# Kernel optimization log

Measured on AMD Instinct MI355X. Metric: run time of the kernel, lower is better.

The kernel has to match this reference:

```python
import jax, jax.numpy as jnp
import numpy as np

N = 50000      # nodes
E = 800000     # edges (avg degree 16)
G = 500        # graphs in batch
D = 128        # emb_dim
ED = 7         # edge_dim
L = 5          # num_layers
C = 10         # num_class
BN_EPS = 1e-5


def _bn(x, g, b, m, v):
    # BatchNorm1d in eval mode: running stats
    return (x - m) * jax.lax.rsqrt(v + BN_EPS) * g + b


def setup_inputs() -> dict:
    key = jax.random.key(0)
    ks = jax.random.split(key, 32)
    f32 = jnp.float32
    edge_attr = jax.random.normal(ks[0], (E, ED), f32)
    edge_index = jax.random.randint(ks[1], (2, E), 0, N)
    batch = jnp.sort(jax.random.randint(ks[2], (N,), 0, G))

    w = lambda k, shp, s: jax.random.normal(k, shp, f32) * s
    s_in = 1.0 / np.sqrt(D)
    node_emb = w(ks[3], (1, D), 1.0)
    edge_W = w(ks[4], (L, ED, D), 1.0 / np.sqrt(ED))
    edge_b = w(ks[5], (L, D), 0.01)
    mlp_W1 = w(ks[6], (L, D, D), s_in)
    mlp_b1 = w(ks[7], (L, D), 0.01)
    mlp_W2 = w(ks[8], (L, D, D), s_in)
    mlp_b2 = w(ks[9], (L, D), 0.01)
    bn1_g = jax.random.uniform(ks[10], (L, D), f32, 0.5, 1.5)
    bn1_b = w(ks[11], (L, D), 0.1)
    bn1_m = w(ks[12], (L, D), 0.1)
    bn1_v = jax.random.uniform(ks[13], (L, D), f32, 0.5, 1.5)
    bn2_g = jax.random.uniform(ks[14], (L, D), f32, 0.5, 1.5)
    bn2_b = w(ks[15], (L, D), 0.1)
    bn2_m = w(ks[16], (L, D), 0.1)
    bn2_v = jax.random.uniform(ks[17], (L, D), f32, 0.5, 1.5)
    head_W1 = w(ks[18], (D, D), s_in)
    head_b1 = w(ks[19], (D,), 0.01)
    head_W2 = w(ks[20], (D, C), s_in)
    head_b2 = w(ks[21], (C,), 0.01)
    return dict(edge_attr=edge_attr, edge_index=edge_index, batch=batch,
                node_emb=node_emb, edge_W=edge_W, edge_b=edge_b,
                mlp_W1=mlp_W1, mlp_b1=mlp_b1, bn1_g=bn1_g, bn1_b=bn1_b,
                bn1_m=bn1_m, bn1_v=bn1_v, mlp_W2=mlp_W2, mlp_b2=mlp_b2,
                bn2_g=bn2_g, bn2_b=bn2_b, bn2_m=bn2_m, bn2_v=bn2_v,
                head_W1=head_W1, head_b1=head_b1, head_W2=head_W2, head_b2=head_b2)


def reference(edge_attr, edge_index, batch, node_emb, edge_W, edge_b,
              mlp_W1, mlp_b1, bn1_g, bn1_b, bn1_m, bn1_v,
              mlp_W2, mlp_b2, bn2_g, bn2_b, bn2_m, bn2_v,
              head_W1, head_b1, head_W2, head_b2):
    src, dst = edge_index[0], edge_index[1]
    # node_emb indexed by zeros -> every node starts with the same row
    x = jnp.broadcast_to(node_emb[0], (N, D))
    for l in range(L):
        # GINEConv: msg_ij = relu(x_j + Lin(edge_attr_ij)); aggr = sum over in-edges
        e = edge_attr @ edge_W[l] + edge_b[l]               # [E, D]
        msg = jax.nn.relu(x[src] + e)                       # gather + add + relu
        agg = jax.ops.segment_sum(msg, dst, num_segments=N) # scatter-add
        h = x + agg                                         # (1 + eps) * x, eps = 0
        # inner MLP: Linear -> BN -> ReLU -> Linear
        h = h @ mlp_W1[l] + mlp_b1[l]
        h = jax.nn.relu(_bn(h, bn1_g[l], bn1_b[l], bn1_m[l], bn1_v[l]))
        h = h @ mlp_W2[l] + mlp_b2[l]
        # outer BN + ReLU (dropout identity in eval)
        x = jax.nn.relu(_bn(h, bn2_g[l], bn2_b[l], bn2_m[l], bn2_v[l]))
    # global mean pool over graphs
    counts = jnp.maximum(jax.ops.segment_sum(jnp.ones((N,), x.dtype), batch, num_segments=G), 1.0)
    g = jax.ops.segment_sum(x, batch, num_segments=G) / counts[:, None]
    # head: Linear -> ReLU -> (Dropout) -> Linear
    h = jax.nn.relu(g @ head_W1 + head_b1)
    return h @ head_W2 + head_b2
```

## Files before the change

kernel.cpp:

```cpp
#include <hip/hip_runtime.h>

#define N_NODES 50000
#define N_PAD   50048
#define N_EDGES 800000
#define N_GRAPHS 500
#define DIM 128
#define EDIM 7
#define LAYERS 5
#define NCLASS 10
#define BN_EPS 1e-5f
#define TM 64
#define AST 264
#define NSB ((N_NODES + 256) / 256)

typedef __attribute__((ext_vector_type(8))) short bf16x8;
typedef __attribute__((ext_vector_type(4))) float f32x4;
typedef _Float16 h2 __attribute__((ext_vector_type(2)));

struct __align__(32) ERec { uint4 ea; int src; int pad0, pad1, pad2; };

__device__ __forceinline__ unsigned short f2bf(float f) {
    unsigned u = __float_as_uint(f);
    u = u + 0x7fffu + ((u >> 16) & 1u);
    return (unsigned short)(u >> 16);
}
__device__ __forceinline__ float bf2f(unsigned short h) {
    return __uint_as_float(((unsigned)h) << 16);
}
__device__ __forceinline__ h2 u2h2(unsigned u) {
    union { unsigned u; h2 h; } c; c.u = u; return c.h;
}
__device__ __forceinline__ unsigned h22u(h2 h) {
    union { h2 h; unsigned u; } c; c.h = h; return c.u;
}
__device__ __forceinline__ unsigned packh2(float a, float b) {
    h2 h; h.x = (_Float16)a; h.y = (_Float16)b;
    return h22u(h);
}


__global__ void zero_ints(int* __restrict__ p, int n) {
    int i = blockIdx.x * 256 + threadIdx.x;
    if (i < n) p[i] = 0;
}

__global__ void hist_kernel(const int* __restrict__ dst, int* __restrict__ deg) {
    int e = blockIdx.x * 256 + threadIdx.x;
    if (e < N_EDGES) atomicAdd(&deg[dst[e]], 1);
}

__global__ __launch_bounds__(256)
void scan1(const int* __restrict__ deg, int* __restrict__ ro, int* __restrict__ bsums) {
    __shared__ int ws[4];
    int t = threadIdx.x;
    int i = blockIdx.x * 256 + t;
    int v = (i < N_NODES) ? deg[i] : 0;
    int lane = t & 63, wv = t >> 6;
    int s = v;
    #pragma unroll
    for (int off = 1; off < 64; off <<= 1) {
        int u = __shfl_up(s, off, 64);
        if (lane >= off) s += u;
    }
    if (lane == 63) ws[wv] = s;
    __syncthreads();
    if (t == 0) {
        int a = 0;
        #pragma unroll
        for (int k = 0; k < 4; ++k) { int x = ws[k]; ws[k] = a; a += x; }
        bsums[blockIdx.x] = a;
    }
    __syncthreads();
    int excl = s - v + ws[wv];
    if (i <= N_NODES) ro[i] = excl;
}

__global__ __launch_bounds__(256)
void scan2(int* __restrict__ bsums) {
    __shared__ int ws[4];
    int t = threadIdx.x;
    int v = (t < NSB) ? bsums[t] : 0;
    int lane = t & 63, wv = t >> 6;
    int s = v;
    #pragma unroll
    for (int off = 1; off < 64; off <<= 1) {
        int u = __shfl_up(s, off, 64);
        if (lane >= off) s += u;
    }
    if (lane == 63) ws[wv] = s;
    __syncthreads();
    if (t == 0) {
        int a = 0;
        #pragma unroll
        for (int k = 0; k < 4; ++k) { int x = ws[k]; ws[k] = a; a += x; }
    }
    __syncthreads();
    if (t < NSB) bsums[t] = s - v + ws[wv];
}

__global__ __launch_bounds__(256)
void scan3(int* __restrict__ ro, const int* __restrict__ bsums, int* __restrict__ cursor) {
    int i = blockIdx.x * 256 + threadIdx.x;
    if (i <= N_NODES) {
        int r = ro[i] + bsums[i >> 8];
        ro[i] = r;
        if (i < N_NODES) cursor[i] = r;
    }
}

__global__ void fill_rec(const int* __restrict__ dst, const int* __restrict__ src,
                         const float* __restrict__ edge_attr,
                         int* __restrict__ cursor, ERec* __restrict__ rec) {
    int e = blockIdx.x * 256 + threadIdx.x;
    if (e < N_EDGES) {
        const float* ap = edge_attr + (size_t)e * EDIM;
        uint4 ea;
        ea.x = packh2(ap[0], ap[1]);
        ea.y = packh2(ap[2], ap[3]);
        ea.z = packh2(ap[4], ap[5]);
        ea.w = packh2(ap[6], 0.f);
        int s = src[e];
        int pos = atomicAdd(&cursor[dst[e]], 1);
        rec[pos].ea = ea;
        rec[pos].src = s;
    }
}


__global__ void init_x(float* __restrict__ x, unsigned short* __restrict__ xb,
                       const float* __restrict__ emb) {
    int i = blockIdx.x * 256 + threadIdx.x;
    if (i < N_NODES * DIM) {
        float v = emb[i & (DIM - 1)];
        x[i] = v;
        xb[i] = f2bf(v);
    }
}

__global__ void prep_w(const float* __restrict__ W1, const float* __restrict__ W2,
                       unsigned short* __restrict__ Wthi, unsigned short* __restrict__ Wtlo) {
    int i = blockIdx.x * 256 + threadIdx.x;
    if (i >= 2 * LAYERS * DIM * DIM) return;
    int m = i >> 14;
    int n = i & 127;
    int k = (i >> 7) & 127;
    const float* W = (m < LAYERS) ? (W1 + (size_t)m * DIM * DIM)
                                  : (W2 + (size_t)(m - LAYERS) * DIM * DIM);
    float v = W[k * DIM + n];
    unsigned short hi = f2bf(v);
    float lo = v - bf2f(hi);
    size_t o = ((size_t)m << 14) + (size_t)n * DIM + k;
    Wthi[o] = hi;
    Wtlo[o] = f2bf(lo);
}


#if __has_builtin(__builtin_amdgcn_fdot2)
#define HAVE_FDOT2 1
#else
#define HAVE_FDOT2 0
#endif

__device__ __forceinline__ void edge_accum2(float& acc0, float& acc1,
                                            uint4 eav, unsigned xv,
                                            const unsigned* Wp0, const unsigned* Wp1,
                                            float b0, float b1) {
    float e0 = b0, e1 = b1;
#if HAVE_FDOT2
    e0 = __builtin_amdgcn_fdot2(u2h2(eav.x), u2h2(Wp0[0]), e0, false);
    e0 = __builtin_amdgcn_fdot2(u2h2(eav.y), u2h2(Wp0[1]), e0, false);
    e0 = __builtin_amdgcn_fdot2(u2h2(eav.z), u2h2(Wp0[2]), e0, false);
    e0 = __builtin_amdgcn_fdot2(u2h2(eav.w), u2h2(Wp0[3]), e0, false);
    e1 = __builtin_amdgcn_fdot2(u2h2(eav.x), u2h2(Wp1[0]), e1, false);
    e1 = __builtin_amdgcn_fdot2(u2h2(eav.y), u2h2(Wp1[1]), e1, false);
    e1 = __builtin_amdgcn_fdot2(u2h2(eav.z), u2h2(Wp1[2]), e1, false);
    e1 = __builtin_amdgcn_fdot2(u2h2(eav.w), u2h2(Wp1[3]), e1, false);
#else
    h2 ea01 = u2h2(eav.x), ea23 = u2h2(eav.y), ea45 = u2h2(eav.z), ea67 = u2h2(eav.w);
    float a[8] = {(float)ea01.x, (float)ea01.y, (float)ea23.x, (float)ea23.y,
                  (float)ea45.x, (float)ea45.y, (float)ea67.x, 0.f};
    #pragma unroll
    for (int kp = 0; kp < 4; ++kp) {
        h2 w0 = u2h2(Wp0[kp]), w1 = u2h2(Wp1[kp]);
        e0 += a[kp * 2] * (float)w0.x + a[kp * 2 + 1] * (float)w0.y;
        e1 += a[kp * 2] * (float)w1.x + a[kp * 2 + 1] * (float)w1.y;
    }
#endif
    acc0 += fmaxf(__uint_as_float(xv << 16)         + e0, 0.f);
    acc1 += fmaxf(__uint_as_float(xv & 0xffff0000u) + e1, 0.f);
}

__global__ __launch_bounds__(256, 8)
void aggregate(const float* __restrict__ x, const unsigned short* __restrict__ xb,
               float* __restrict__ h,
               const ERec* __restrict__ rec,
               const int* __restrict__ row_off,
               const float* __restrict__ eW, const float* __restrict__ eb) {
    int t = threadIdx.x;
    int wv = __builtin_amdgcn_readfirstlane(t >> 6);
    int lane = t & 63;
    int c0 = lane * 2;
    int n = blockIdx.x * 4 + wv;

    unsigned Wp0[4], Wp1[4];
    #pragma unroll
    for (int kp = 0; kp < 4; ++kp) {
        float w00 = eW[(kp * 2) * DIM + c0];
        float w01 = (kp * 2 + 1 < EDIM) ? eW[(kp * 2 + 1) * DIM + c0] : 0.f;
        float w10 = eW[(kp * 2) * DIM + c0 + 1];
        float w11 = (kp * 2 + 1 < EDIM) ? eW[(kp * 2 + 1) * DIM + c0 + 1] : 0.f;
        Wp0[kp] = packh2(w00, w01);
        Wp1[kp] = packh2(w10, w11);
    }
    float b0 = eb[c0], b1 = eb[c0 + 1];
    #pragma unroll
    for (int k = 0; k < 4; ++k) asm volatile("" : "+v"(Wp0[k]), "+v"(Wp1[k]));
    asm volatile("" : "+v"(b0), "+v"(b1));

    float acc0 = x[(size_t)n * DIM + c0];
    float acc1 = x[(size_t)n * DIM + c0 + 1];
    int idx = row_off[n], end = row_off[n + 1];

    for (; idx + 8 <= end; idx += 8) {
        ERec r[8];
        #pragma unroll
        for (int j = 0; j < 8; ++j) r[j] = rec[idx + j];
        unsigned xv[8];
        #pragma unroll
        for (int j = 0; j < 8; ++j)
            xv[j] = *reinterpret_cast<const unsigned*>(xb + (size_t)r[j].src * DIM + c0);
        #pragma unroll
        for (int j = 0; j < 8; ++j)
            edge_accum2(acc0, acc1, r[j].ea, xv[j], Wp0, Wp1, b0, b1);
    }
    for (; idx < end; ++idx) {
        ERec r0 = rec[idx];
        unsigned xv0 = *reinterpret_cast<const unsigned*>(xb + (size_t)r0.src * DIM + c0);
        edge_accum2(acc0, acc1, r0.ea, xv0, Wp0, Wp1, b0, b1);
    }

    float2 o; o.x = acc0; o.y = acc1;
    *reinterpret_cast<float2*>(h + (size_t)n * DIM + c0) = o;
}


__global__ __launch_bounds__(256)
void gemm2x(const float* __restrict__ in, float* __restrict__ outx,
            unsigned short* __restrict__ xb_out,
            const unsigned short* __restrict__ W1hi, const unsigned short* __restrict__ W1lo,
            const unsigned short* __restrict__ W2hi, const unsigned short* __restrict__ W2lo,
            const float* __restrict__ b1,
            const float* __restrict__ bn1g, const float* __restrict__ bn1b,
            const float* __restrict__ bn1m, const float* __restrict__ bn1v,
            const float* __restrict__ b2,
            const float* __restrict__ bn2g, const float* __restrict__ bn2b,
            const float* __restrict__ bn2m, const float* __restrict__ bn2v) {
    __shared__ __align__(16) unsigned short A2[TM * AST];
    int t = threadIdx.x;
    int r0 = blockIdx.x * TM;
    int w = t >> 6;
    int lane = t & 63;
    int q = lane >> 4;
    int l16 = lane & 15;

    bf16x8 bh[2][4], bl[2][4];
    #pragma unroll
    for (int nt = 0; nt < 2; ++nt) {
        int n = w * 32 + nt * 16 + l16;
        const bf16x8* gh = reinterpret_cast<const bf16x8*>(W1hi + (size_t)n * DIM);
        const bf16x8* gl = reinterpret_cast<const bf16x8*>(W1lo + (size_t)n * DIM);
        #pragma unroll
        for (int kc = 0; kc < 4; ++kc) {
            bh[nt][kc] = gh[kc * 4 + q];
            bl[nt][kc] = gl[kc * 4 + q];
        }
    }

    #pragma unroll
    for (int i = 0; i < 8; ++i) {
        int idx = t + i * 256;
        int row = idx >> 5;
        int kp = (idx & 31) * 4;
        float4 v = reinterpret_cast<const float4*>(in + (size_t)r0 * DIM)[idx];
        unsigned short h0 = f2bf(v.x), h1 = f2bf(v.y), h2_ = f2bf(v.z), h3 = f2bf(v.w);
        ushort4 hv; hv.x = h0; hv.y = h1; hv.z = h2_; hv.w = h3;
        ushort4 lv;
        lv.x = f2bf(v.x - bf2f(h0)); lv.y = f2bf(v.y - bf2f(h1));
        lv.z = f2bf(v.z - bf2f(h2_)); lv.w = f2bf(v.w - bf2f(h3));
        *reinterpret_cast<ushort4*>(&A2[row * AST + kp]) = hv;
        *reinterpret_cast<ushort4*>(&A2[row * AST + 128 + kp]) = lv;
    }
    __syncthreads();

    f32x4 acc[4][2];
    #pragma unroll
    for (int mt = 0; mt < 4; ++mt)
        #pragma unroll
        for (int nt = 0; nt < 2; ++nt)
            acc[mt][nt] = (f32x4){0.f, 0.f, 0.f, 0.f};

    #pragma unroll
    for (int kc = 0; kc < 4; ++kc) {
        bf16x8 ahi[4], alo[4];
        #pragma unroll
        for (int mt = 0; mt < 4; ++mt) {
            ahi[mt] = *reinterpret_cast<const bf16x8*>(&A2[(mt * 16 + l16) * AST + kc * 32 + q * 8]);
            alo[mt] = *reinterpret_cast<const bf16x8*>(&A2[(mt * 16 + l16) * AST + 128 + kc * 32 + q * 8]);
        }
        #pragma unroll
        for (int mt = 0; mt < 4; ++mt)
            #pragma unroll
            for (int nt = 0; nt < 2; ++nt) {
                acc[mt][nt] = __builtin_amdgcn_mfma_f32_16x16x32_bf16(ahi[mt], bh[nt][kc], acc[mt][nt], 0, 0, 0);
                acc[mt][nt] = __builtin_amdgcn_mfma_f32_16x16x32_bf16(ahi[mt], bl[nt][kc], acc[mt][nt], 0, 0, 0);
                acc[mt][nt] = __builtin_amdgcn_mfma_f32_16x16x32_bf16(alo[mt], bh[nt][kc], acc[mt][nt], 0, 0, 0);
            }
    }
    __syncthreads();

    #pragma unroll
    for (int nt = 0; nt < 2; ++nt) {
        int n = w * 32 + nt * 16 + l16;
        const bf16x8* gh = reinterpret_cast<const bf16x8*>(W2hi + (size_t)n * DIM);
        const bf16x8* gl = reinterpret_cast<const bf16x8*>(W2lo + (size_t)n * DIM);
        #pragma unroll
        for (int kc = 0; kc < 4; ++kc) {
            bh[nt][kc] = gh[kc * 4 + q];
            bl[nt][kc] = gl[kc * 4 + q];
        }
    }

    #pragma unroll
    for (int nt = 0; nt < 2; ++nt) {
        int col = w * 32 + nt * 16 + l16;
        float bias = b1[col];
        float sc = bn1g[col] * rsqrtf(bn1v[col] + BN_EPS);
        float sh = bn1b[col] - bn1m[col] * sc;
        #pragma unroll
        for (int mt = 0; mt < 4; ++mt) {
            #pragma unroll
            for (int r = 0; r < 4; ++r) {
                int rowl = mt * 16 + q * 4 + r;
                float o = fmaxf((acc[mt][nt][r] + bias) * sc + sh, 0.f);
                unsigned short hi = f2bf(o);
                A2[rowl * AST + col] = hi;
                A2[rowl * AST + 128 + col] = f2bf(o - bf2f(hi));
            }
        }
    }
    __syncthreads();

    #pragma unroll
    for (int mt = 0; mt < 4; ++mt)
        #pragma unroll
        for (int nt = 0; nt < 2; ++nt)
            acc[mt][nt] = (f32x4){0.f, 0.f, 0.f, 0.f};

    #pragma unroll
    for (int kc = 0; kc < 4; ++kc) {
        bf16x8 ahi[4], alo[4];
        #pragma unroll
        for (int mt = 0; mt < 4; ++mt) {
            ahi[mt] = *reinterpret_cast<const bf16x8*>(&A2[(mt * 16 + l16) * AST + kc * 32 + q * 8]);
            alo[mt] = *reinterpret_cast<const bf16x8*>(&A2[(mt * 16 + l16) * AST + 128 + kc * 32 + q * 8]);
        }
        #pragma unroll
        for (int mt = 0; mt < 4; ++mt)
            #pragma unroll
            for (int nt = 0; nt < 2; ++nt) {
                acc[mt][nt] = __builtin_amdgcn_mfma_f32_16x16x32_bf16(ahi[mt], bh[nt][kc], acc[mt][nt], 0, 0, 0);
                acc[mt][nt] = __builtin_amdgcn_mfma_f32_16x16x32_bf16(ahi[mt], bl[nt][kc], acc[mt][nt], 0, 0, 0);
                acc[mt][nt] = __builtin_amdgcn_mfma_f32_16x16x32_bf16(alo[mt], bh[nt][kc], acc[mt][nt], 0, 0, 0);
            }
    }

    #pragma unroll
    for (int nt = 0; nt < 2; ++nt) {
        int col = w * 32 + nt * 16 + l16;
        float bias = b2[col];
        float sc = bn2g[col] * rsqrtf(bn2v[col] + BN_EPS);
        float sh = bn2b[col] - bn2m[col] * sc;
        #pragma unroll
        for (int mt = 0; mt < 4; ++mt) {
            #pragma unroll
            for (int r = 0; r < 4; ++r) {
                int row = r0 + mt * 16 + q * 4 + r;
                float o = fmaxf((acc[mt][nt][r] + bias) * sc + sh, 0.f);
                outx[(size_t)row * DIM + col] = o;
                xb_out[(size_t)row * DIM + col] = f2bf(o);
            }
        }
    }
}


__global__ __launch_bounds__(256)
void pool_kernel(const float* __restrict__ x, const int* __restrict__ batch,
                 float* __restrict__ g) {
    __shared__ float sh[256];
    __shared__ int sb[2];
    int gid = blockIdx.x;
    int t = threadIdx.x;
    if (t < 2) {
        int tgt = gid + t;
        int lo = 0, hi = N_NODES;
        while (lo < hi) { int mid = (lo + hi) >> 1; if (batch[mid] < tgt) lo = mid + 1; else hi = mid; }
        sb[t] = lo;
    }
    __syncthreads();
    int lo = sb[0], hi = sb[1];
    int d = t & 127, half = t >> 7;
    float a = 0.f;
    for (int n = lo + half; n < hi; n += 2) a += x[(size_t)n * DIM + d];
    sh[t] = a;
    __syncthreads();
    if (t < DIM) {
        float cnt = fmaxf((float)(hi - lo), 1.f);
        g[gid * DIM + t] = (sh[t] + sh[t + 128]) / cnt;
    }
}


__global__ __launch_bounds__(128)
void head1_kernel(const float* __restrict__ g, const float* __restrict__ W1,
                  const float* __restrict__ b1, float* __restrict__ h1) {
    __shared__ float gs[DIM];
    int gid = blockIdx.x, c = threadIdx.x;
    gs[c] = g[gid * DIM + c];
    __syncthreads();
    float acc = b1[c];
    for (int k = 0; k < DIM; ++k) acc += gs[k] * W1[k * DIM + c];
    h1[gid * DIM + c] = fmaxf(acc, 0.f);
}

__global__ __launch_bounds__(64)
void head2_kernel(const float* __restrict__ h1, const float* __restrict__ W2,
                  const float* __restrict__ b2, float* __restrict__ out) {
    __shared__ float hs[DIM];
    int gid = blockIdx.x;
    int t = threadIdx.x;
    hs[t] = h1[gid * DIM + t];
    hs[t + 64] = h1[gid * DIM + t + 64];
    __syncthreads();
    if (t < NCLASS) {
        float acc = b2[t];
        for (int k = 0; k < DIM; ++k) acc += hs[k] * W2[k * NCLASS + t];
        out[gid * NCLASS + t] = acc;
    }
}


extern "C" void kernel_launch(void* const* d_in, const int* in_sizes, int n_in,
                              void* d_out, int out_size, void* d_ws, size_t ws_size,
                              hipStream_t stream) {
    const float* edge_attr = (const float*)d_in[0];
    const int*   edge_index = (const int*)d_in[1];
    const int*   batch = (const int*)d_in[2];
    const float* node_emb = (const float*)d_in[3];
    const float* edge_W = (const float*)d_in[4];
    const float* edge_b = (const float*)d_in[5];
    const float* mlp_W1 = (const float*)d_in[6];
    const float* mlp_b1 = (const float*)d_in[7];
    const float* bn1_g = (const float*)d_in[8];
    const float* bn1_b = (const float*)d_in[9];
    const float* bn1_m = (const float*)d_in[10];
    const float* bn1_v = (const float*)d_in[11];
    const float* mlp_W2 = (const float*)d_in[12];
    const float* mlp_b2 = (const float*)d_in[13];
    const float* bn2_g = (const float*)d_in[14];
    const float* bn2_b = (const float*)d_in[15];
    const float* bn2_m = (const float*)d_in[16];
    const float* bn2_v = (const float*)d_in[17];
    const float* head_W1 = (const float*)d_in[18];
    const float* head_b1 = (const float*)d_in[19];
    const float* head_W2 = (const float*)d_in[20];
    const float* head_b2 = (const float*)d_in[21];
    float* out = (float*)d_out;

    const int* src = edge_index;
    const int* dst = edge_index + N_EDGES;

    size_t off = 0;
    auto carve = [&](size_t bytes) {
        void* p = (char*)d_ws + off;
        off += (bytes + 255) & ~(size_t)255;
        return p;
    };
    float* x            = (float*)carve((size_t)N_PAD * DIM * 4);
    unsigned short* xb  = (unsigned short*)carve((size_t)N_PAD * DIM * 2);
    float* h            = (float*)carve((size_t)N_PAD * DIM * 4);
    ERec* rec           = (ERec*)carve((size_t)N_EDGES * sizeof(ERec));
    unsigned short* Wthi = (unsigned short*)carve((size_t)2 * LAYERS * DIM * DIM * 2);
    unsigned short* Wtlo = (unsigned short*)carve((size_t)2 * LAYERS * DIM * DIM * 2);
    int* deg      = (int*)carve((size_t)N_NODES * 4);
    int* row_off  = (int*)carve((size_t)(N_NODES + 1) * 4);
    int* cursor   = (int*)carve((size_t)N_NODES * 4);
    int* bsums    = (int*)carve((size_t)NSB * 4);
    float* gbuf   = (float*)carve((size_t)N_GRAPHS * DIM * 4);
    float* h1buf  = (float*)carve((size_t)N_GRAPHS * DIM * 4);
    (void)ws_size;

    zero_ints<<<(N_NODES + 255) / 256, 256, 0, stream>>>(deg, N_NODES);
    hist_kernel<<<(N_EDGES + 255) / 256, 256, 0, stream>>>(dst, deg);
    scan1<<<NSB, 256, 0, stream>>>(deg, row_off, bsums);
    scan2<<<1, 256, 0, stream>>>(bsums);
    scan3<<<NSB, 256, 0, stream>>>(row_off, bsums, cursor);
    fill_rec<<<(N_EDGES + 255) / 256, 256, 0, stream>>>(dst, src, edge_attr, cursor, rec);

    init_x<<<(N_NODES * DIM + 255) / 256, 256, 0, stream>>>(x, xb, node_emb);
    prep_w<<<(2 * LAYERS * DIM * DIM + 255) / 256, 256, 0, stream>>>(mlp_W1, mlp_W2, Wthi, Wtlo);

    const int gemm_blocks = N_PAD / TM;
    for (int l = 0; l < LAYERS; ++l) {
        aggregate<<<N_NODES / 4, 256, 0, stream>>>(
            x, xb, h, rec, row_off,
            edge_W + (size_t)l * EDIM * DIM, edge_b + (size_t)l * DIM);
        gemm2x<<<gemm_blocks, 256, 0, stream>>>(
            h, x, xb,
            Wthi + ((size_t)l << 14), Wtlo + ((size_t)l << 14),
            Wthi + ((size_t)(LAYERS + l) << 14), Wtlo + ((size_t)(LAYERS + l) << 14),
            mlp_b1 + (size_t)l * DIM,
            bn1_g + (size_t)l * DIM, bn1_b + (size_t)l * DIM,
            bn1_m + (size_t)l * DIM, bn1_v + (size_t)l * DIM,
            mlp_b2 + (size_t)l * DIM,
            bn2_g + (size_t)l * DIM, bn2_b + (size_t)l * DIM,
            bn2_m + (size_t)l * DIM, bn2_v + (size_t)l * DIM);
    }

    pool_kernel<<<N_GRAPHS, 256, 0, stream>>>(x, batch, gbuf);
    head1_kernel<<<N_GRAPHS, 128, 0, stream>>>(gbuf, head_W1, head_b1, h1buf);
    head2_kernel<<<N_GRAPHS, 64, 0, stream>>>(h1buf, head_W2, head_b2, out);
}
```

Before: 622.5 us.

## Fuse edge aggregation into the per-layer MLP GEMM kernel

Merges the aggregate and gemm2x kernels into one layer_fused kernel. Each wave aggregates 16 destination nodes and writes the hi/lo bf16 split straight into the shared-memory A tile, then the block runs the two-layer MLP. This removes the fp32 h intermediate round trip through global memory and one launch per layer. The bf16 node buffer is now ping-ponged so blocks still reading the previous layer are not overwritten. The cost is far fewer blocks (one per 64 rows) and lower occupancy for a latency-bound gather, plus per-wave load imbalance across nodes.

Measured after the change: 1.001 ms. 60.7% more time.

```diff
diff --git a/kernel.cpp b/kernel.cpp
--- a/kernel.cpp
+++ b/kernel.cpp
@@ -190,75 +190,26 @@
     acc1 += fmaxf(__uint_as_float(xv & 0xffff0000u) + e1, 0.f);
 }
 
-__global__ __launch_bounds__(256, 8)
-void aggregate(const float* __restrict__ x, const unsigned short* __restrict__ xb,
-               float* __restrict__ h,
-               const ERec* __restrict__ rec,
-               const int* __restrict__ row_off,
-               const float* __restrict__ eW, const float* __restrict__ eb) {
-    int t = threadIdx.x;
-    int wv = __builtin_amdgcn_readfirstlane(t >> 6);
-    int lane = t & 63;
-    int c0 = lane * 2;
-    int n = blockIdx.x * 4 + wv;
-
-    unsigned Wp0[4], Wp1[4];
-    #pragma unroll
-    for (int kp = 0; kp < 4; ++kp) {
-        float w00 = eW[(kp * 2) * DIM + c0];
-        float w01 = (kp * 2 + 1 < EDIM) ? eW[(kp * 2 + 1) * DIM + c0] : 0.f;
-        float w10 = eW[(kp * 2) * DIM + c0 + 1];
-        float w11 = (kp * 2 + 1 < EDIM) ? eW[(kp * 2 + 1) * DIM + c0 + 1] : 0.f;
-        Wp0[kp] = packh2(w00, w01);
-        Wp1[kp] = packh2(w10, w11);
-    }
-    float b0 = eb[c0], b1 = eb[c0 + 1];
-    #pragma unroll
-    for (int k = 0; k < 4; ++k) asm volatile("" : "+v"(Wp0[k]), "+v"(Wp1[k]));
-    asm volatile("" : "+v"(b0), "+v"(b1));
-
-    float acc0 = x[(size_t)n * DIM + c0];
-    float acc1 = x[(size_t)n * DIM + c0 + 1];
-    int idx = row_off[n], end = row_off[n + 1];
-
-    for (; idx + 8 <= end; idx += 8) {
-        ERec r[8];
-        #pragma unroll
-        for (int j = 0; j < 8; ++j) r[j] = rec[idx + j];
-        unsigned xv[8];
-        #pragma unroll
-        for (int j = 0; j < 8; ++j)
-            xv[j] = *reinterpret_cast<const unsigned*>(xb + (size_t)r[j].src * DIM + c0);
-        #pragma unroll
-        for (int j = 0; j < 8; ++j)
-            edge_accum2(acc0, acc1, r[j].ea, xv[j], Wp0, Wp1, b0, b1);
-    }
-    for (; idx < end; ++idx) {
-        ERec r0 = rec[idx];
-        unsigned xv0 = *reinterpret_cast<const unsigned*>(xb + (size_t)r0.src * DIM + c0);
-        edge_accum2(acc0, acc1, r0.ea, xv0, Wp0, Wp1, b0, b1);
-    }
-
-    float2 o; o.x = acc0; o.y = acc1;
-    *reinterpret_cast<float2*>(h + (size_t)n * DIM + c0) = o;
-}
-
-
 __global__ __launch_bounds__(256)
-void gemm2x(const float* __restrict__ in, float* __restrict__ outx,
-            unsigned short* __restrict__ xb_out,
-            const unsigned short* __restrict__ W1hi, const unsigned short* __restrict__ W1lo,
-            const unsigned short* __restrict__ W2hi, const unsigned short* __restrict__ W2lo,
-            const float* __restrict__ b1,
-            const float* __restrict__ bn1g, const float* __restrict__ bn1b,
-            const float* __restrict__ bn1m, const float* __restrict__ bn1v,
-            const float* __restrict__ b2,
-            const float* __restrict__ bn2g, const float* __restrict__ bn2b,
-            const float* __restrict__ bn2m, const float* __restrict__ bn2v) {
+void layer_fused(float* __restrict__ x,
+                 const unsigned short* __restrict__ xb_in,
+                 unsigned short* __restrict__ xb_out,
+                 const ERec* __restrict__ rec,
+                 const int* __restrict__ row_off,
+                 const float* __restrict__ eW, const float* __restrict__ eb,
+                 const unsigned short* __restrict__ W1hi, const unsigned short* __restrict__ W1lo,
+                 const unsigned short* __restrict__ W2hi, const unsigned short* __restrict__ W2lo,
+                 const float* __restrict__ b1,
+                 const float* __restrict__ bn1g, const float* __restrict__ bn1b,
+                 const float* __restrict__ bn1m, const float* __restrict__ bn1v,
+                 const float* __restrict__ b2,
+                 const float* __restrict__ bn2g, const float* __restrict__ bn2b,
+                 const float* __restrict__ bn2m, const float* __restrict__ bn2v) {
     __shared__ __align__(16) unsigned short A2[TM * AST];
     int t = threadIdx.x;
     int r0 = blockIdx.x * TM;
     int w = t >> 6;
+    int wv16 = __builtin_amdgcn_readfirstlane(w) * 16;
     int lane = t & 63;
     int q = lane >> 4;
     int l16 = lane & 15;
@@ -276,19 +227,55 @@
         }
     }
 
-    #pragma unroll
-    for (int i = 0; i < 8; ++i) {
-        int idx = t + i * 256;
-        int row = idx >> 5;
-        int kp = (idx & 31) * 4;
-        float4 v = reinterpret_cast<const float4*>(in + (size_t)r0 * DIM)[idx];
-        unsigned short h0 = f2bf(v.x), h1 = f2bf(v.y), h2_ = f2bf(v.z), h3 = f2bf(v.w);
-        ushort4 hv; hv.x = h0; hv.y = h1; hv.z = h2_; hv.w = h3;
-        ushort4 lv;
-        lv.x = f2bf(v.x - bf2f(h0)); lv.y = f2bf(v.y - bf2f(h1));
-        lv.z = f2bf(v.z - bf2f(h2_)); lv.w = f2bf(v.w - bf2f(h3));
-        *reinterpret_cast<ushort4*>(&A2[row * AST + kp]) = hv;
-        *reinterpret_cast<ushort4*>(&A2[row * AST + 128 + kp]) = lv;
+    {
+        int c0 = lane * 2;
+        unsigned Wp0[4], Wp1[4];
+        #pragma unroll
+        for (int kp = 0; kp < 4; ++kp) {
+            float w00 = eW[(kp * 2) * DIM + c0];
+            float w01 = (kp * 2 + 1 < EDIM) ? eW[(kp * 2 + 1) * DIM + c0] : 0.f;
+            float w10 = eW[(kp * 2) * DIM + c0 + 1];
+            float w11 = (kp * 2 + 1 < EDIM) ? eW[(kp * 2 + 1) * DIM + c0 + 1] : 0.f;
+            Wp0[kp] = packh2(w00, w01);
+            Wp1[kp] = packh2(w10, w11);
+        }
+        float b0 = eb[c0], b1v = eb[c0 + 1];
+        #pragma unroll
+        for (int k = 0; k < 4; ++k) asm volatile("" : "+v"(Wp0[k]), "+v"(Wp1[k]));
+        asm volatile("" : "+v"(b0), "+v"(b1v));
+
+        for (int i = 0; i < 16; ++i) {
+            int n = r0 + wv16 + i;
+            if (n < N_NODES) {
+                float acc0 = x[(size_t)n * DIM + c0];
+                float acc1 = x[(size_t)n * DIM + c0 + 1];
+                int idx = row_off[n], end = row_off[n + 1];
+                for (; idx + 8 <= end; idx += 8) {
+                    ERec r[8];
+                    #pragma unroll
+                    for (int j = 0; j < 8; ++j) r[j] = rec[idx + j];
+                    unsigned xv[8];
+                    #pragma unroll
+                    for (int j = 0; j < 8; ++j)
+                        xv[j] = *reinterpret_cast<const unsigned*>(xb_in + (size_t)r[j].src * DIM + c0);
+                    #pragma unroll
+                    for (int j = 0; j < 8; ++j)
+                        edge_accum2(acc0, acc1, r[j].ea, xv[j], Wp0, Wp1, b0, b1v);
+                }
+                for (; idx < end; ++idx) {
+                    ERec r0e = rec[idx];
+                    unsigned xv0 = *reinterpret_cast<const unsigned*>(xb_in + (size_t)r0e.src * DIM + c0);
+                    edge_accum2(acc0, acc1, r0e.ea, xv0, Wp0, Wp1, b0, b1v);
+                }
+                int rowl = wv16 + i;
+                unsigned short h0 = f2bf(acc0), h1 = f2bf(acc1);
+                *reinterpret_cast<unsigned*>(&A2[rowl * AST + c0]) =
+                    (unsigned)h0 | ((unsigned)h1 << 16);
+                unsigned short l0 = f2bf(acc0 - bf2f(h0)), l1 = f2bf(acc1 - bf2f(h1));
+                *reinterpret_cast<unsigned*>(&A2[rowl * AST + 128 + c0]) =
+                    (unsigned)l0 | ((unsigned)l1 << 16);
+            }
+        }
     }
     __syncthreads();
 
@@ -386,7 +373,7 @@
             for (int r = 0; r < 4; ++r) {
                 int row = r0 + mt * 16 + q * 4 + r;
                 float o = fmaxf((acc[mt][nt][r] + bias) * sc + sh, 0.f);
-                outx[(size_t)row * DIM + col] = o;
+                x[(size_t)row * DIM + col] = o;
                 xb_out[(size_t)row * DIM + col] = f2bf(o);
             }
         }
@@ -487,8 +474,8 @@
         return p;
     };
     float* x            = (float*)carve((size_t)N_PAD * DIM * 4);
-    unsigned short* xb  = (unsigned short*)carve((size_t)N_PAD * DIM * 2);
-    float* h            = (float*)carve((size_t)N_PAD * DIM * 4);
+    unsigned short* xba = (unsigned short*)carve((size_t)N_PAD * DIM * 2);
+    unsigned short* xbb = (unsigned short*)carve((size_t)N_PAD * DIM * 2);
     ERec* rec           = (ERec*)carve((size_t)N_EDGES * sizeof(ERec));
     unsigned short* Wthi = (unsigned short*)carve((size_t)2 * LAYERS * DIM * DIM * 2);
     unsigned short* Wtlo = (unsigned short*)carve((size_t)2 * LAYERS * DIM * DIM * 2);
@@ -507,16 +494,16 @@
     scan3<<<NSB, 256, 0, stream>>>(row_off, bsums, cursor);
     fill_rec<<<(N_EDGES + 255) / 256, 256, 0, stream>>>(dst, src, edge_attr, cursor, rec);
 
-    init_x<<<(N_NODES * DIM + 255) / 256, 256, 0, stream>>>(x, xb, node_emb);
+    init_x<<<(N_NODES * DIM + 255) / 256, 256, 0, stream>>>(x, xba, node_emb);
     prep_w<<<(2 * LAYERS * DIM * DIM + 255) / 256, 256, 0, stream>>>(mlp_W1, mlp_W2, Wthi, Wtlo);
 
     const int gemm_blocks = N_PAD / TM;
     for (int l = 0; l < LAYERS; ++l) {
-        aggregate<<<N_NODES / 4, 256, 0, stream>>>(
-            x, xb, h, rec, row_off,
-            edge_W + (size_t)l * EDIM * DIM, edge_b + (size_t)l * DIM);
-        gemm2x<<<gemm_blocks, 256, 0, stream>>>(
-            h, x, xb,
+        unsigned short* xb_in  = (l & 1) ? xbb : xba;
+        unsigned short* xb_out = (l & 1) ? xba : xbb;
+        layer_fused<<<gemm_blocks, 256, 0, stream>>>(
+            x, xb_in, xb_out, rec, row_off,
+            edge_W + (size_t)l * EDIM * DIM, edge_b + (size_t)l * DIM,
             Wthi + ((size_t)l << 14), Wtlo + ((size_t)l << 14),
             Wthi + ((size_t)(LAYERS + l) << 14), Wtlo + ((size_t)(LAYERS + l) << 14),
             mlp_b1 + (size_t)l * DIM,
```
